# Kernel tuning notes

Hardware: AMD Instinct MI355X
Metric: run time of the kernel (lower is better)

## Reference

```python
import jax, jax.numpy as jnp
import numpy as np

N_A = 100000
N_B = 100000


def _mean_agg(x_src, src, dst, n_dst):
    # gather source features along edges, mean-aggregate into destination nodes
    msgs = x_src[src]                                        # [E, d]
    s = jax.ops.segment_sum(msgs, dst, num_segments=n_dst)   # [n_dst, d]
    ones = jnp.ones((dst.shape[0], 1), dtype=x_src.dtype)
    cnt = jax.ops.segment_sum(ones, dst, num_segments=n_dst)
    return s / jnp.maximum(cnt, jnp.asarray(1.0, x_src.dtype))


def setup_inputs() -> dict:
    key = jax.random.key(0)
    ks = jax.random.split(key, 13)
    E = 1200000
    d = 64
    return {
        "x_A": jax.random.normal(ks[0], (N_A, d), jnp.float32),
        "x_B": jax.random.normal(ks[1], (N_B, d), jnp.float32),
        "Wn": jax.random.normal(ks[2], (2, 3, d, d), jnp.float32) * 0.1,
        "Wr": jax.random.normal(ks[3], (2, 3, d, d), jnp.float32) * 0.1,
        "b": jax.random.normal(ks[4], (2, 3, d), jnp.float32) * 0.1,
        "W_out": jax.random.normal(ks[5], (d, d), jnp.float32) * 0.1,
        "b_out": jax.random.normal(ks[6], (d,), jnp.float32) * 0.1,
        "src0": jax.random.randint(ks[7], (E,), 0, N_A, jnp.int64 if jax.config.jax_enable_x64 else jnp.int32),
        "dst0": jax.random.randint(ks[8], (E,), 0, N_B, jnp.int32),
        "src1": jax.random.randint(ks[9], (E,), 0, N_B, jnp.int32),
        "dst1": jax.random.randint(ks[10], (E,), 0, N_A, jnp.int32),
        "src2": jax.random.randint(ks[11], (E,), 0, N_A, jnp.int32),
        "dst2": jax.random.randint(ks[12], (E,), 0, N_A, jnp.int32),
    }


def reference(x_A, x_B, Wn, Wr, b, W_out, b_out,
              src0, dst0, src1, dst1, src2, dst2):
    # Two stacked heterogeneous conv layers (SAGEConv-style per edge type,
    # summed across edge types per destination node type), then Linear+ReLU head.
    for l in range(2):
        m0 = _mean_agg(x_A, src0, dst0, N_B)  # A -> B
        m1 = _mean_agg(x_B, src1, dst1, N_A)  # B -> A
        m2 = _mean_agg(x_A, src2, dst2, N_A)  # A -> A
        new_B = m0 @ Wn[l, 0] + x_B @ Wr[l, 0] + b[l, 0]
        new_A = (m1 @ Wn[l, 1] + x_A @ Wr[l, 1] + b[l, 1]
                 + m2 @ Wn[l, 2] + x_A @ Wr[l, 2] + b[l, 2])
        x_A, x_B = new_A, new_B
    out_A = jax.nn.relu(x_A @ W_out + b_out)
    out_B = jax.nn.relu(x_B @ W_out + b_out)
    return jnp.concatenate([out_A, out_B], axis=0)  # [N_A + N_B, d]
```

## Files before the change

kernel.cpp:

```cpp
#include <hip/hip_runtime.h>
#include <hip/hip_bf16.h>

typedef __bf16 bf16_t;
typedef unsigned short u16;
typedef short short8 __attribute__((ext_vector_type(8)));
typedef float f32x4 __attribute__((ext_vector_type(4)));

#define BSHIFT 9
#define CAP 8192
#define TILE 4096

__device__ inline short f2bs(float v) {
    bf16_t h = (bf16_t)v;
    return __builtin_bit_cast(short, h);
}
__device__ inline float uif(unsigned u) { return __builtin_bit_cast(float, u); }

__global__ __launch_bounds__(256) void prep_convert(
    const float* __restrict__ xA, const float* __restrict__ xB,
    const float* __restrict__ Wn, const float* __restrict__ Wr,
    const float* __restrict__ Wout,
    u16* __restrict__ plane0, u16* __restrict__ wh, int NA, int NB) {
    int nA4 = NA * 16, nB4 = NB * 16;
    int bA = (nA4 + 255) / 256, bB = (nB4 + 255) / 256;
    int bi = blockIdx.x;
    int tid = threadIdx.x;
    if (bi < bA + bB) {
        const float* in = (bi < bA) ? xA : xB;
        u16* out = (bi < bA) ? plane0 : plane0 + (size_t)NA * 64;
        int i = (bi < bA ? bi : bi - bA) * 256 + tid;
        int n4 = (bi < bA) ? nA4 : nB4;
        if (i >= n4) return;
        float4 v = ((const float4*)in)[i];
        u16 o[4];
        o[0] = (u16)f2bs(v.x); o[1] = (u16)f2bs(v.y);
        o[2] = (u16)f2bs(v.z); o[3] = (u16)f2bs(v.w);
        *(uint2*)(out + (size_t)i * 4) = *(uint2*)o;
        return;
    }
    int mat = bi - bA - bB;
    u16* dstp = wh + (size_t)mat * 4096;
    for (int i = tid; i < 4096; i += 256) {
        int k = i >> 6, n = i & 63;
        float v;
        if (mat < 6) v = Wn[(size_t)mat * 4096 + i];
        else if (mat < 8) v = Wr[(size_t)((mat - 6) * 3 + 0) * 4096 + i];
        else if (mat < 10) v = Wr[(size_t)((mat - 8) * 3 + 1) * 4096 + i]
                             + Wr[(size_t)((mat - 8) * 3 + 2) * 4096 + i];
        else v = Wout[i];
        dstp[n * 64 + k] = (u16)f2bs(v);
    }
}

__global__ __launch_bounds__(256) void init_cursor(int* __restrict__ gcursor, int K) {
    int i = blockIdx.x * 256 + threadIdx.x;
    if (i < K) gcursor[i] = i * CAP;
}

__global__ __launch_bounds__(256) void partition_kernel(
    const int* __restrict__ s0, const int* __restrict__ d0,
    const int* __restrict__ s1, const int* __restrict__ d1,
    const int* __restrict__ s2, const int* __restrict__ d2,
    int* __restrict__ gcursor, int* __restrict__ pairs,
    int NB, int NA, int E, int total) {
    __shared__ int hist[1024];
    __shared__ int gbase[1024];
    int tid = threadIdx.x;
    for (int tile = blockIdx.x * TILE; tile < total; tile += gridDim.x * TILE) {
        for (int i = tid; i < 1024; i += 256) hist[i] = 0;
        __syncthreads();
        int mybkt[16], mypk[16], myrank[16];
#pragma unroll
        for (int j = 0; j < 16; j++) {
            int idx = tile + j * 256 + tid;
            int g = -1, s = 0;
            if (idx < total) {
                if (idx < E) { s = s0[idx]; g = d0[idx]; }
                else if (idx < 2 * E) { s = s1[idx - E]; g = NB + d1[idx - E]; }
                else { s = s2[idx - 2 * E]; g = NB + NA + d2[idx - 2 * E]; }
            }
            if (g >= 0) {
                mybkt[j] = g >> BSHIFT;
                mypk[j] = ((g & ((1 << BSHIFT) - 1)) << 17) | s;
                myrank[j] = atomicAdd(&hist[mybkt[j]], 1);
            } else mybkt[j] = -1;
        }
        __syncthreads();
        for (int bq = tid; bq < 1024; bq += 256) {
            int c = hist[bq];
            if (c) gbase[bq] = atomicAdd(&gcursor[bq], c);
        }
        __syncthreads();
#pragma unroll
        for (int j = 0; j < 16; j++) {
            if (mybkt[j] >= 0)
                pairs[gbase[mybkt[j]] + myrank[j]] = mypk[j];
        }
        __syncthreads();
    }
}

__global__ __launch_bounds__(512) void bucket_fill(const int* __restrict__ pairs,
                                                   const int* __restrict__ gcursor,
                                                   int* __restrict__ off_s,
                                                   int* __restrict__ off_e,
                                                   int* __restrict__ colidx, int M) {
    int b = blockIdx.x;
    int gb = b << BSHIFT;
    __shared__ int cnt[512], cur[512], wsum[8];
    int tid = threadIdx.x;
    int lane = tid & 63, w = tid >> 6;
    int p0 = b * CAP, p1 = gcursor[b];
    cnt[tid] = 0;
    __syncthreads();
    for (int e = p0 + tid; e < p1; e += 512)
        atomicAdd(&cnt[(unsigned)pairs[e] >> 17], 1);
    __syncthreads();
    int v = cnt[tid];
    int x = v;
#pragma unroll
    for (int off = 1; off < 64; off <<= 1) {
        int n = __shfl_up(x, off);
        if (lane >= off) x += n;
    }
    if (lane == 63) wsum[w] = x;
    __syncthreads();
    if (tid == 0) {
        int s = 0;
#pragma unroll
        for (int i = 0; i < 8; i++) { int t = wsum[i]; wsum[i] = s; s += t; }
    }
    __syncthreads();
    int excl = x - v + wsum[w];
    cur[tid] = excl;
    int g = gb + tid;
    if (g < M) { off_s[g] = p0 + excl; off_e[g] = p0 + excl + v; }
    __syncthreads();
    for (int e = p0 + tid; e < p1; e += 512) {
        int p = pairs[e];
        int pos = atomicAdd(&cur[(unsigned)p >> 17], 1);
        colidx[p0 + pos] = p & 0x1FFFF;
    }
}

__device__ __forceinline__ void acc8(uint4 u, f32x4& a0, f32x4& a1) {
    a0[0] += uif(u.x << 16); a0[1] += uif(u.x & 0xFFFF0000u);
    a0[2] += uif(u.y << 16); a0[3] += uif(u.y & 0xFFFF0000u);
    a1[0] += uif(u.z << 16); a1[1] += uif(u.z & 0xFFFF0000u);
    a1[2] += uif(u.w << 16); a1[3] += uif(u.w & 0xFFFF0000u);
}

__global__ __launch_bounds__(256) void gather_all(const u16* __restrict__ plane,
                                                  const int* __restrict__ colidx,
                                                  const int* __restrict__ off_s,
                                                  const int* __restrict__ off_e,
                                                  u16* __restrict__ meanB,
                                                  u16* __restrict__ meanA1,
                                                  u16* __restrict__ meanA2,
                                                  int NB, int NA) {
    int wid = (blockIdx.x * 256 + threadIdx.x) >> 6;
    int lane = threadIdx.x & 63;
    int oct = lane >> 3, fl = lane & 7;
    int M = NB + 2 * NA;
    int grow = wid * 8 + oct;
    if (grow >= M) return;

    const char* tab;
    u16* outp;
    int orow;
    if (grow < NB) { tab = (const char*)plane; outp = meanB; orow = grow; }
    else if (grow < NB + NA) { tab = (const char*)(plane + (size_t)NA * 64); outp = meanA1; orow = grow - NB; }
    else { tab = (const char*)plane; outp = meanA2; orow = grow - NB - NA; }

    int s0 = off_s[grow], s1 = off_e[grow];
    unsigned fo = (unsigned)(fl << 4);
    f32x4 a0 = {0.f, 0.f, 0.f, 0.f}, a1 = {0.f, 0.f, 0.f, 0.f};

    int e = s0;
    if (e + 3 < s1) {
        int c0 = colidx[e], c1 = colidx[e + 1];
        int c2 = colidx[e + 2], c3 = colidx[e + 3];
        while (e + 7 < s1) {
            uint4 u0 = *(const uint4*)(tab + (((unsigned)c0 << 7) | fo));
            uint4 u1 = *(const uint4*)(tab + (((unsigned)c1 << 7) | fo));
            uint4 u2 = *(const uint4*)(tab + (((unsigned)c2 << 7) | fo));
            uint4 u3 = *(const uint4*)(tab + (((unsigned)c3 << 7) | fo));
            c0 = colidx[e + 4]; c1 = colidx[e + 5];
            c2 = colidx[e + 6]; c3 = colidx[e + 7];
            acc8(u0, a0, a1); acc8(u1, a0, a1);
            acc8(u2, a0, a1); acc8(u3, a0, a1);
            e += 4;
        }
        {
            uint4 u0 = *(const uint4*)(tab + (((unsigned)c0 << 7) | fo));
            uint4 u1 = *(const uint4*)(tab + (((unsigned)c1 << 7) | fo));
            uint4 u2 = *(const uint4*)(tab + (((unsigned)c2 << 7) | fo));
            uint4 u3 = *(const uint4*)(tab + (((unsigned)c3 << 7) | fo));
            acc8(u0, a0, a1); acc8(u1, a0, a1);
            acc8(u2, a0, a1); acc8(u3, a0, a1);
            e += 4;
        }
    }
    for (; e < s1; ++e) {
        int c = colidx[e];
        uint4 u = *(const uint4*)(tab + (((unsigned)c << 7) | fo));
        acc8(u, a0, a1);
    }

    float inv = 1.0f / fmaxf((float)(s1 - s0), 1.0f);
    u16 o[8];
#pragma unroll
    for (int i = 0; i < 4; i++) o[i] = (u16)f2bs(a0[i] * inv);
#pragma unroll
    for (int i = 0; i < 4; i++) o[4 + i] = (u16)f2bs(a1[i] * inv);
    *(uint4*)(outp + (size_t)orow * 64 + fl * 8) = *(uint4*)o;
}

template <int NM, int RELU, int OUTF32>
__device__ __forceinline__ void lin_body(
    const u16* __restrict__ m0, const u16* __restrict__ m1,
    const u16* __restrict__ x,
    const u16* __restrict__ Wm0t, const u16* __restrict__ Wm1t,
    const u16* __restrict__ Wxt,
    const float* __restrict__ bias0, const float* __restrict__ bias1,
    void* __restrict__ outv, int nrows, int blk) {
    const int lane = threadIdx.x & 63;
    const int wave = threadIdx.x >> 6;
    const int row0 = blk * 64 + wave * 16;
    if (row0 >= nrows) return;
    const int r = lane & 15;
    const int q = lane >> 4;

    short8 wm0f[2][4], wm1f[2][4], wxf[2][4];
#pragma unroll
    for (int ks = 0; ks < 2; ks++) {
#pragma unroll
        for (int t = 0; t < 4; t++) {
            size_t widx = (size_t)(t * 16 + r) * 64 + ks * 32 + q * 8;
            if (NM >= 1) wm0f[ks][t] = *(const short8*)(Wm0t + widx);
            if (NM >= 2) wm1f[ks][t] = *(const short8*)(Wm1t + widx);
            wxf[ks][t] = *(const short8*)(Wxt + widx);
        }
    }

    f32x4 acc[4];
#pragma unroll
    for (int t = 0; t < 4; t++) {
        float bv = bias0[t * 16 + r];
        if (bias1) bv += bias1[t * 16 + r];
        acc[t][0] = bv; acc[t][1] = bv; acc[t][2] = bv; acc[t][3] = bv;
    }

    const int arow = row0 + r;
    const bool avalid = arow < nrows;
    short8 zf;
#pragma unroll
    for (int j = 0; j < 8; j++) zf[j] = 0;

    if (NM >= 1) {
#pragma unroll
        for (int ks = 0; ks < 2; ks++) {
            short8 af = avalid ? *(const short8*)(m0 + (size_t)arow * 64 + ks * 32 + q * 8) : zf;
#pragma unroll
            for (int t = 0; t < 4; t++)
                acc[t] = __builtin_amdgcn_mfma_f32_16x16x32_bf16(af, wm0f[ks][t], acc[t], 0, 0, 0);
        }
    }
    if (NM >= 2) {
#pragma unroll
        for (int ks = 0; ks < 2; ks++) {
            short8 af = avalid ? *(const short8*)(m1 + (size_t)arow * 64 + ks * 32 + q * 8) : zf;
#pragma unroll
            for (int t = 0; t < 4; t++)
                acc[t] = __builtin_amdgcn_mfma_f32_16x16x32_bf16(af, wm1f[ks][t], acc[t], 0, 0, 0);
        }
    }
#pragma unroll
    for (int ks = 0; ks < 2; ks++) {
        short8 xf = avalid ? *(const short8*)(x + (size_t)arow * 64 + ks * 32 + q * 8) : zf;
#pragma unroll
        for (int t = 0; t < 4; t++)
            acc[t] = __builtin_amdgcn_mfma_f32_16x16x32_bf16(xf, wxf[ks][t], acc[t], 0, 0, 0);
    }

#pragma unroll
    for (int t = 0; t < 4; t++) {
#pragma unroll
        for (int rr = 0; rr < 4; rr++) {
            int row = row0 + q * 4 + rr;
            if (row < nrows) {
                float v = acc[t][rr];
                if (RELU) v = fmaxf(v, 0.0f);
                if (OUTF32) ((float*)outv)[(size_t)row * 64 + t * 16 + r] = v;
                else ((u16*)outv)[(size_t)row * 64 + t * 16 + r] = (u16)f2bs(v);
            }
        }
    }
}

__global__ __launch_bounds__(256) void layer_kernel(
    const u16* __restrict__ plane_in, u16* __restrict__ plane_out,
    const u16* __restrict__ meanB, const u16* __restrict__ meanA1,
    const u16* __restrict__ meanA2, const u16* __restrict__ wh,
    const float* __restrict__ bvec, int l, int NA, int NB, int blocksB) {
    if ((int)blockIdx.x < blocksB) {
        lin_body<1, 0, 0>(meanB, nullptr, plane_in + (size_t)NA * 64,
                          wh + (size_t)(l * 3 + 0) * 4096, nullptr,
                          wh + (size_t)(6 + l) * 4096,
                          bvec + (size_t)(l * 3 + 0) * 64, nullptr,
                          plane_out + (size_t)NA * 64, NB, blockIdx.x);
    } else {
        lin_body<2, 0, 0>(meanA1, meanA2, plane_in,
                          wh + (size_t)(l * 3 + 1) * 4096, wh + (size_t)(l * 3 + 2) * 4096,
                          wh + (size_t)(8 + l) * 4096,
                          bvec + (size_t)(l * 3 + 1) * 64, bvec + (size_t)(l * 3 + 2) * 64,
                          plane_out, NA, blockIdx.x - blocksB);
    }
}

__global__ __launch_bounds__(256) void head_kernel(
    const u16* __restrict__ plane_in, const u16* __restrict__ wh,
    const float* __restrict__ b_out, float* __restrict__ out, int nrows) {
    lin_body<0, 1, 1>(nullptr, nullptr, plane_in,
                      nullptr, nullptr, wh + (size_t)10 * 4096,
                      b_out, nullptr, out, nrows, blockIdx.x);
}

extern "C" void kernel_launch(void* const* d_in, const int* in_sizes, int n_in,
                              void* d_out, int out_size, void* d_ws, size_t ws_size,
                              hipStream_t stream) {
    const float* xA_in = (const float*)d_in[0];
    const float* xB_in = (const float*)d_in[1];
    const float* Wn = (const float*)d_in[2];
    const float* Wr = (const float*)d_in[3];
    const float* b = (const float*)d_in[4];
    const float* W_out = (const float*)d_in[5];
    const float* b_out = (const float*)d_in[6];
    const int* src0 = (const int*)d_in[7];
    const int* dst0 = (const int*)d_in[8];
    const int* src1 = (const int*)d_in[9];
    const int* dst1 = (const int*)d_in[10];
    const int* src2 = (const int*)d_in[11];
    const int* dst2 = (const int*)d_in[12];

    const int NA = in_sizes[0] / 64;
    const int NB = in_sizes[1] / 64;
    const int E = in_sizes[7];
    const int M = NB + NA + NA;
    const int total = 3 * E;
    const int K = (M + (1 << BSHIFT) - 1) >> BSHIFT;

    const size_t PL = (size_t)(NA + NB) * 64;
    u16* plane[2];
    plane[0] = (u16*)d_ws;
    plane[1] = plane[0] + PL;
    u16* wh     = plane[1] + PL;
    u16* meanB  = wh + 11 * 4096;
    u16* meanA1 = meanB + (size_t)NB * 64;
    u16* meanA2 = meanA1 + (size_t)NA * 64;
    int* gcursor= (int*)(meanA2 + (size_t)NA * 64);
    int* off_s  = gcursor + 1024;
    int* off_e  = off_s + M;
    int* colidx = off_e + M;
    int* pairs  = (int*)meanB;

    int bA = (NA * 16 + 255) / 256, bB = (NB * 16 + 255) / 256;
    prep_convert<<<bA + bB + 11, 256, 0, stream>>>(
        xA_in, xB_in, Wn, Wr, W_out, plane[0], wh, NA, NB);

    init_cursor<<<(K + 255) / 256, 256, 0, stream>>>(gcursor, K);
    int ntiles = (total + TILE - 1) / TILE;
    partition_kernel<<<ntiles, 256, 0, stream>>>(src0, dst0, src1, dst1, src2, dst2,
                                                 gcursor, pairs, NB, NA, E, total);
    bucket_fill<<<K, 512, 0, stream>>>(pairs, gcursor, off_s, off_e, colidx, M);

    const int blocksB = (NB + 63) / 64;
    const int blocksA = (NA + 63) / 64;
    int p = 0;
    for (int l = 0; l < 2; l++) {
        gather_all<<<(M + 31) / 32, 256, 0, stream>>>(plane[p], colidx, off_s, off_e,
                                                      meanB, meanA1, meanA2, NB, NA);
        layer_kernel<<<blocksB + blocksA, 256, 0, stream>>>(
            plane[p], plane[1 - p], meanB, meanA1, meanA2, wh, b, l, NA, NB, blocksB);
        p = 1 - p;
    }

    head_kernel<<<(NA + NB + 63) / 64, 256, 0, stream>>>(
        plane[p], wh, b_out, (float*)d_out, NA + NB);
}
```

Before: 427.2 us.

## Fuse head into layer-2 kernel, merge cursor init, widen partition blocks

The output head linear+ReLU now runs inside the second layer kernel. Each wave writes its layer-2 tile to shared memory and applies W_out right there, so the full bf16 plane is neither written to nor re-read from global memory, and one launch is removed. Cursor initialisation is folded into prep_convert as an extra block, which drops another launch. The partition kernel now uses 1024-thread blocks with larger tiles, one histogram bin per thread. Weight fragments are loaded inline inside the MFMA loop instead of being preloaded, which changes register pressure and load scheduling.

```diff
diff --git a/kernel.cpp b/kernel.cpp
--- a/kernel.cpp
+++ b/kernel.cpp
@@ -8,7 +8,7 @@
 
 #define BSHIFT 9
 #define CAP 8192
-#define TILE 4096
+#define TILE 16384
 
 __device__ inline short f2bs(float v) {
     bf16_t h = (bf16_t)v;
@@ -20,7 +20,8 @@
     const float* __restrict__ xA, const float* __restrict__ xB,
     const float* __restrict__ Wn, const float* __restrict__ Wr,
     const float* __restrict__ Wout,
-    u16* __restrict__ plane0, u16* __restrict__ wh, int NA, int NB) {
+    u16* __restrict__ plane0, u16* __restrict__ wh,
+    int* __restrict__ gcursor, int NA, int NB, int K) {
     int nA4 = NA * 16, nB4 = NB * 16;
     int bA = (nA4 + 255) / 256, bB = (nB4 + 255) / 256;
     int bi = blockIdx.x;
@@ -38,26 +39,25 @@
         *(uint2*)(out + (size_t)i * 4) = *(uint2*)o;
         return;
     }
-    int mat = bi - bA - bB;
-    u16* dstp = wh + (size_t)mat * 4096;
-    for (int i = tid; i < 4096; i += 256) {
-        int k = i >> 6, n = i & 63;
-        float v;
-        if (mat < 6) v = Wn[(size_t)mat * 4096 + i];
-        else if (mat < 8) v = Wr[(size_t)((mat - 6) * 3 + 0) * 4096 + i];
-        else if (mat < 10) v = Wr[(size_t)((mat - 8) * 3 + 1) * 4096 + i]
-                             + Wr[(size_t)((mat - 8) * 3 + 2) * 4096 + i];
-        else v = Wout[i];
-        dstp[n * 64 + k] = (u16)f2bs(v);
-    }
-}
-
-__global__ __launch_bounds__(256) void init_cursor(int* __restrict__ gcursor, int K) {
-    int i = blockIdx.x * 256 + threadIdx.x;
-    if (i < K) gcursor[i] = i * CAP;
-}
-
-__global__ __launch_bounds__(256) void partition_kernel(
+    if (bi < bA + bB + 11) {
+        int mat = bi - bA - bB;
+        u16* dstp = wh + (size_t)mat * 4096;
+        for (int i = tid; i < 4096; i += 256) {
+            int k = i >> 6, n = i & 63;
+            float v;
+            if (mat < 6) v = Wn[(size_t)mat * 4096 + i];
+            else if (mat < 8) v = Wr[(size_t)((mat - 6) * 3 + 0) * 4096 + i];
+            else if (mat < 10) v = Wr[(size_t)((mat - 8) * 3 + 1) * 4096 + i]
+                                 + Wr[(size_t)((mat - 8) * 3 + 2) * 4096 + i];
+            else v = Wout[i];
+            dstp[n * 64 + k] = (u16)f2bs(v);
+        }
+        return;
+    }
+    for (int i = tid; i < K; i += 256) gcursor[i] = i * CAP;
+}
+
+__global__ __launch_bounds__(1024) void partition_kernel(
     const int* __restrict__ s0, const int* __restrict__ d0,
     const int* __restrict__ s1, const int* __restrict__ d1,
     const int* __restrict__ s2, const int* __restrict__ d2,
@@ -67,12 +67,12 @@
     __shared__ int gbase[1024];
     int tid = threadIdx.x;
     for (int tile = blockIdx.x * TILE; tile < total; tile += gridDim.x * TILE) {
-        for (int i = tid; i < 1024; i += 256) hist[i] = 0;
+        hist[tid] = 0;
         __syncthreads();
         int mybkt[16], mypk[16], myrank[16];
 #pragma unroll
         for (int j = 0; j < 16; j++) {
-            int idx = tile + j * 256 + tid;
+            int idx = tile + j * 1024 + tid;
             int g = -1, s = 0;
             if (idx < total) {
                 if (idx < E) { s = s0[idx]; g = d0[idx]; }
@@ -86,9 +86,9 @@
             } else mybkt[j] = -1;
         }
         __syncthreads();
-        for (int bq = tid; bq < 1024; bq += 256) {
-            int c = hist[bq];
-            if (c) gbase[bq] = atomicAdd(&gcursor[bq], c);
+        {
+            int c = hist[tid];
+            if (c) gbase[tid] = atomicAdd(&gcursor[tid], c);
         }
         __syncthreads();
 #pragma unroll
@@ -216,14 +216,15 @@
     *(uint4*)(outp + (size_t)orow * 64 + fl * 8) = *(uint4*)o;
 }
 
-template <int NM, int RELU, int OUTF32>
+
+template <int NM>
 __device__ __forceinline__ void lin_body(
     const u16* __restrict__ m0, const u16* __restrict__ m1,
     const u16* __restrict__ x,
     const u16* __restrict__ Wm0t, const u16* __restrict__ Wm1t,
     const u16* __restrict__ Wxt,
     const float* __restrict__ bias0, const float* __restrict__ bias1,
-    void* __restrict__ outv, int nrows, int blk) {
+    u16* __restrict__ outv, int nrows, int blk) {
     const int lane = threadIdx.x & 63;
     const int wave = threadIdx.x >> 6;
     const int row0 = blk * 64 + wave * 16;
@@ -231,23 +232,11 @@
     const int r = lane & 15;
     const int q = lane >> 4;
 
-    short8 wm0f[2][4], wm1f[2][4], wxf[2][4];
-#pragma unroll
-    for (int ks = 0; ks < 2; ks++) {
-#pragma unroll
-        for (int t = 0; t < 4; t++) {
-            size_t widx = (size_t)(t * 16 + r) * 64 + ks * 32 + q * 8;
-            if (NM >= 1) wm0f[ks][t] = *(const short8*)(Wm0t + widx);
-            if (NM >= 2) wm1f[ks][t] = *(const short8*)(Wm1t + widx);
-            wxf[ks][t] = *(const short8*)(Wxt + widx);
-        }
-    }
-
     f32x4 acc[4];
 #pragma unroll
     for (int t = 0; t < 4; t++) {
         float bv = bias0[t * 16 + r];
-        if (bias1) bv += bias1[t * 16 + r];
+        if (NM >= 2) bv += bias1[t * 16 + r];
         acc[t][0] = bv; acc[t][1] = bv; acc[t][2] = bv; acc[t][3] = bv;
     }
 
@@ -257,30 +246,20 @@
 #pragma unroll
     for (int j = 0; j < 8; j++) zf[j] = 0;
 
-    if (NM >= 1) {
-#pragma unroll
-        for (int ks = 0; ks < 2; ks++) {
-            short8 af = avalid ? *(const short8*)(m0 + (size_t)arow * 64 + ks * 32 + q * 8) : zf;
-#pragma unroll
-            for (int t = 0; t < 4; t++)
-                acc[t] = __builtin_amdgcn_mfma_f32_16x16x32_bf16(af, wm0f[ks][t], acc[t], 0, 0, 0);
-        }
-    }
-    if (NM >= 2) {
-#pragma unroll
-        for (int ks = 0; ks < 2; ks++) {
-            short8 af = avalid ? *(const short8*)(m1 + (size_t)arow * 64 + ks * 32 + q * 8) : zf;
-#pragma unroll
-            for (int t = 0; t < 4; t++)
-                acc[t] = __builtin_amdgcn_mfma_f32_16x16x32_bf16(af, wm1f[ks][t], acc[t], 0, 0, 0);
-        }
-    }
 #pragma unroll
     for (int ks = 0; ks < 2; ks++) {
+        short8 af = avalid ? *(const short8*)(m0 + (size_t)arow * 64 + ks * 32 + q * 8) : zf;
         short8 xf = avalid ? *(const short8*)(x + (size_t)arow * 64 + ks * 32 + q * 8) : zf;
-#pragma unroll
-        for (int t = 0; t < 4; t++)
-            acc[t] = __builtin_amdgcn_mfma_f32_16x16x32_bf16(xf, wxf[ks][t], acc[t], 0, 0, 0);
+        short8 bf_;
+        if (NM >= 2) bf_ = avalid ? *(const short8*)(m1 + (size_t)arow * 64 + ks * 32 + q * 8) : zf;
+#pragma unroll
+        for (int t = 0; t < 4; t++) {
+            size_t widx = (size_t)(t * 16 + r) * 64 + ks * 32 + q * 8;
+            acc[t] = __builtin_amdgcn_mfma_f32_16x16x32_bf16(af, *(const short8*)(Wm0t + widx), acc[t], 0, 0, 0);
+            if (NM >= 2)
+                acc[t] = __builtin_amdgcn_mfma_f32_16x16x32_bf16(bf_, *(const short8*)(Wm1t + widx), acc[t], 0, 0, 0);
+            acc[t] = __builtin_amdgcn_mfma_f32_16x16x32_bf16(xf, *(const short8*)(Wxt + widx), acc[t], 0, 0, 0);
+        }
     }
 
 #pragma unroll
@@ -288,42 +267,128 @@
 #pragma unroll
         for (int rr = 0; rr < 4; rr++) {
             int row = row0 + q * 4 + rr;
-            if (row < nrows) {
-                float v = acc[t][rr];
-                if (RELU) v = fmaxf(v, 0.0f);
-                if (OUTF32) ((float*)outv)[(size_t)row * 64 + t * 16 + r] = v;
-                else ((u16*)outv)[(size_t)row * 64 + t * 16 + r] = (u16)f2bs(v);
-            }
-        }
-    }
-}
-
-__global__ __launch_bounds__(256) void layer_kernel(
+            if (row < nrows)
+                outv[(size_t)row * 64 + t * 16 + r] = (u16)f2bs(acc[t][rr]);
+        }
+    }
+}
+
+__global__ __launch_bounds__(256) void layer1_kernel(
     const u16* __restrict__ plane_in, u16* __restrict__ plane_out,
     const u16* __restrict__ meanB, const u16* __restrict__ meanA1,
     const u16* __restrict__ meanA2, const u16* __restrict__ wh,
-    const float* __restrict__ bvec, int l, int NA, int NB, int blocksB) {
+    const float* __restrict__ bvec, int NA, int NB, int blocksB) {
     if ((int)blockIdx.x < blocksB) {
-        lin_body<1, 0, 0>(meanB, nullptr, plane_in + (size_t)NA * 64,
-                          wh + (size_t)(l * 3 + 0) * 4096, nullptr,
-                          wh + (size_t)(6 + l) * 4096,
-                          bvec + (size_t)(l * 3 + 0) * 64, nullptr,
-                          plane_out + (size_t)NA * 64, NB, blockIdx.x);
+        lin_body<1>(meanB, nullptr, plane_in + (size_t)NA * 64,
+                    wh + (size_t)0 * 4096, nullptr, wh + (size_t)6 * 4096,
+                    bvec + (size_t)0 * 64, nullptr,
+                    plane_out + (size_t)NA * 64, NB, blockIdx.x);
     } else {
-        lin_body<2, 0, 0>(meanA1, meanA2, plane_in,
-                          wh + (size_t)(l * 3 + 1) * 4096, wh + (size_t)(l * 3 + 2) * 4096,
-                          wh + (size_t)(8 + l) * 4096,
-                          bvec + (size_t)(l * 3 + 1) * 64, bvec + (size_t)(l * 3 + 2) * 64,
-                          plane_out, NA, blockIdx.x - blocksB);
-    }
-}
-
-__global__ __launch_bounds__(256) void head_kernel(
-    const u16* __restrict__ plane_in, const u16* __restrict__ wh,
-    const float* __restrict__ b_out, float* __restrict__ out, int nrows) {
-    lin_body<0, 1, 1>(nullptr, nullptr, plane_in,
-                      nullptr, nullptr, wh + (size_t)10 * 4096,
-                      b_out, nullptr, out, nrows, blockIdx.x);
+        lin_body<2>(meanA1, meanA2, plane_in,
+                    wh + (size_t)1 * 4096, wh + (size_t)2 * 4096, wh + (size_t)8 * 4096,
+                    bvec + (size_t)1 * 64, bvec + (size_t)2 * 64,
+                    plane_out, NA, blockIdx.x - blocksB);
+    }
+}
+
+template <int NM>
+__device__ __forceinline__ void lin_body_head(
+    const u16* __restrict__ m0, const u16* __restrict__ m1,
+    const u16* __restrict__ x,
+    const u16* __restrict__ Wm0t, const u16* __restrict__ Wm1t,
+    const u16* __restrict__ Wxt,
+    const float* __restrict__ bias0, const float* __restrict__ bias1,
+    const u16* __restrict__ Woutt, const float* __restrict__ b_out,
+    float* __restrict__ out, int nrows, int blk) {
+    const int lane = threadIdx.x & 63;
+    const int wave = threadIdx.x >> 6;
+    const int row0 = blk * 64 + wave * 16;
+    const int r = lane & 15;
+    const int q = lane >> 4;
+    const int arow = row0 + r;
+    const bool avalid = (row0 < nrows) && (arow < nrows);
+
+    __shared__ __align__(16) u16 xt[4][16][72];
+
+    f32x4 acc[4];
+#pragma unroll
+    for (int t = 0; t < 4; t++) {
+        float bv = bias0[t * 16 + r];
+        if (NM >= 2) bv += bias1[t * 16 + r];
+        acc[t][0] = bv; acc[t][1] = bv; acc[t][2] = bv; acc[t][3] = bv;
+    }
+
+    short8 zf;
+#pragma unroll
+    for (int j = 0; j < 8; j++) zf[j] = 0;
+
+#pragma unroll
+    for (int ks = 0; ks < 2; ks++) {
+        short8 af = avalid ? *(const short8*)(m0 + (size_t)arow * 64 + ks * 32 + q * 8) : zf;
+        short8 xf = avalid ? *(const short8*)(x + (size_t)arow * 64 + ks * 32 + q * 8) : zf;
+        short8 bf_;
+        if (NM >= 2) bf_ = avalid ? *(const short8*)(m1 + (size_t)arow * 64 + ks * 32 + q * 8) : zf;
+#pragma unroll
+        for (int t = 0; t < 4; t++) {
+            size_t widx = (size_t)(t * 16 + r) * 64 + ks * 32 + q * 8;
+            acc[t] = __builtin_amdgcn_mfma_f32_16x16x32_bf16(af, *(const short8*)(Wm0t + widx), acc[t], 0, 0, 0);
+            if (NM >= 2)
+                acc[t] = __builtin_amdgcn_mfma_f32_16x16x32_bf16(bf_, *(const short8*)(Wm1t + widx), acc[t], 0, 0, 0);
+            acc[t] = __builtin_amdgcn_mfma_f32_16x16x32_bf16(xf, *(const short8*)(Wxt + widx), acc[t], 0, 0, 0);
+        }
+    }
+
+#pragma unroll
+    for (int t = 0; t < 4; t++)
+#pragma unroll
+        for (int rr = 0; rr < 4; rr++)
+            xt[wave][q * 4 + rr][t * 16 + r] = (u16)f2bs(acc[t][rr]);
+    __syncthreads();
+
+    f32x4 hacc[4];
+#pragma unroll
+    for (int t = 0; t < 4; t++) {
+        float bv = b_out[t * 16 + r];
+        hacc[t][0] = bv; hacc[t][1] = bv; hacc[t][2] = bv; hacc[t][3] = bv;
+    }
+#pragma unroll
+    for (int ks = 0; ks < 2; ks++) {
+        short8 yf = *(const short8*)&xt[wave][r][ks * 32 + q * 8];
+#pragma unroll
+        for (int t = 0; t < 4; t++) {
+            size_t widx = (size_t)(t * 16 + r) * 64 + ks * 32 + q * 8;
+            hacc[t] = __builtin_amdgcn_mfma_f32_16x16x32_bf16(yf, *(const short8*)(Woutt + widx), hacc[t], 0, 0, 0);
+        }
+    }
+#pragma unroll
+    for (int t = 0; t < 4; t++) {
+#pragma unroll
+        for (int rr = 0; rr < 4; rr++) {
+            int row = row0 + q * 4 + rr;
+            if (row < nrows)
+                out[(size_t)row * 64 + t * 16 + r] = fmaxf(hacc[t][rr], 0.0f);
+        }
+    }
+}
+
+__global__ __launch_bounds__(256) void layer2_head_kernel(
+    const u16* __restrict__ plane_in,
+    const u16* __restrict__ meanB, const u16* __restrict__ meanA1,
+    const u16* __restrict__ meanA2, const u16* __restrict__ wh,
+    const float* __restrict__ bvec, const float* __restrict__ b_out,
+    float* __restrict__ out, int NA, int NB, int blocksB) {
+    const u16* Woutt = wh + (size_t)10 * 4096;
+    if ((int)blockIdx.x < blocksB) {
+        lin_body_head<1>(meanB, nullptr, plane_in + (size_t)NA * 64,
+                         wh + (size_t)3 * 4096, nullptr, wh + (size_t)7 * 4096,
+                         bvec + (size_t)3 * 64, nullptr,
+                         Woutt, b_out, out + (size_t)NA * 64, NB, blockIdx.x);
+    } else {
+        lin_body_head<2>(meanA1, meanA2, plane_in,
+                         wh + (size_t)4 * 4096, wh + (size_t)5 * 4096, wh + (size_t)9 * 4096,
+                         bvec + (size_t)4 * 64, bvec + (size_t)5 * 64,
+                         Woutt, b_out, out, NA, blockIdx.x - blocksB);
+    }
 }
 
 extern "C" void kernel_launch(void* const* d_in, const int* in_sizes, int n_in,
@@ -365,26 +430,23 @@
     int* pairs  = (int*)meanB;
 
     int bA = (NA * 16 + 255) / 256, bB = (NB * 16 + 255) / 256;
-    prep_convert<<<bA + bB + 11, 256, 0, stream>>>(
-        xA_in, xB_in, Wn, Wr, W_out, plane[0], wh, NA, NB);
-
-    init_cursor<<<(K + 255) / 256, 256, 0, stream>>>(gcursor, K);
+    prep_convert<<<bA + bB + 11 + 1, 256, 0, stream>>>(
+        xA_in, xB_in, Wn, Wr, W_out, plane[0], wh, gcursor, NA, NB, K);
+
     int ntiles = (total + TILE - 1) / TILE;
-    partition_kernel<<<ntiles, 256, 0, stream>>>(src0, dst0, src1, dst1, src2, dst2,
-                                                 gcursor, pairs, NB, NA, E, total);
+    partition_kernel<<<ntiles, 1024, 0, stream>>>(src0, dst0, src1, dst1, src2, dst2,
+                                                  gcursor, pairs, NB, NA, E, total);
     bucket_fill<<<K, 512, 0, stream>>>(pairs, gcursor, off_s, off_e, colidx, M);
 
     const int blocksB = (NB + 63) / 64;
     const int blocksA = (NA + 63) / 64;
-    int p = 0;
-    for (int l = 0; l < 2; l++) {
-        gather_all<<<(M + 31) / 32, 256, 0, stream>>>(plane[p], colidx, off_s, off_e,
-                                                      meanB, meanA1, meanA2, NB, NA);
-        layer_kernel<<<blocksB + blocksA, 256, 0, stream>>>(
-            plane[p], plane[1 - p], meanB, meanA1, meanA2, wh, b, l, NA, NB, blocksB);
-        p = 1 - p;
-    }
-
-    head_kernel<<<(NA + NB + 63) / 64, 256, 0, stream>>>(
-        plane[p], wh, b_out, (float*)d_out, NA + NB);
-}
+    gather_all<<<(M + 31) / 32, 256, 0, stream>>>(plane[0], colidx, off_s, off_e,
+                                                  meanB, meanA1, meanA2, NB, NA);
+    layer1_kernel<<<blocksB + blocksA, 256, 0, stream>>>(
+        plane[0], plane[1], meanB, meanA1, meanA2, wh, b, NA, NB, blocksB);
+
+    gather_all<<<(M + 31) / 32, 256, 0, stream>>>(plane[1], colidx, off_s, off_e,
+                                                  meanB, meanA1, meanA2, NB, NA);
+    layer2_head_kernel<<<blocksB + blocksA, 256, 0, stream>>>(
+        plane[1], meanB, meanA1, meanA2, wh, b, b_out, (float*)d_out, NA, NB, blocksB);
+}
```

Result: faster. 414.4 us (-3.0%).

## Fold output head into layer-2 weights and fuse init into prep kernel

Applied to the files above, without the earlier changes.

Precomputes the products of the layer-2 weights with W_out and the matching combined biases, so the second layer writes the ReLU head output directly and the separate head kernel and its intermediate plane round trip go away. The cursor init and bias folding move into the prep kernel, which removes one launch. The partition kernel switches to 1024-thread blocks with larger tiles, and lin_body now loads weight fragments inside the MFMA loop instead of preloading them into registers. The folded weights are rounded to bf16 after the product, which shifts numerics slightly.

```diff
diff --git a/kernel.cpp b/kernel.cpp
--- a/kernel.cpp
+++ b/kernel.cpp
@@ -8,7 +8,7 @@
 
 #define BSHIFT 9
 #define CAP 8192
-#define TILE 4096
+#define TILE 16384
 
 __device__ inline short f2bs(float v) {
     bf16_t h = (bf16_t)v;
@@ -19,8 +19,11 @@
 __global__ __launch_bounds__(256) void prep_convert(
     const float* __restrict__ xA, const float* __restrict__ xB,
     const float* __restrict__ Wn, const float* __restrict__ Wr,
-    const float* __restrict__ Wout,
-    u16* __restrict__ plane0, u16* __restrict__ wh, int NA, int NB) {
+    const float* __restrict__ Wout, const float* __restrict__ b,
+    const float* __restrict__ b_out,
+    u16* __restrict__ plane0, u16* __restrict__ wh,
+    int* __restrict__ gcursor, float* __restrict__ biasC,
+    int NA, int NB, int K) {
     int nA4 = NA * 16, nB4 = NB * 16;
     int bA = (nA4 + 255) / 256, bB = (nB4 + 255) / 256;
     int bi = blockIdx.x;
@@ -38,26 +41,60 @@
         *(uint2*)(out + (size_t)i * 4) = *(uint2*)o;
         return;
     }
-    int mat = bi - bA - bB;
-    u16* dstp = wh + (size_t)mat * 4096;
-    for (int i = tid; i < 4096; i += 256) {
-        int k = i >> 6, n = i & 63;
-        float v;
-        if (mat < 6) v = Wn[(size_t)mat * 4096 + i];
-        else if (mat < 8) v = Wr[(size_t)((mat - 6) * 3 + 0) * 4096 + i];
-        else if (mat < 10) v = Wr[(size_t)((mat - 8) * 3 + 1) * 4096 + i]
-                             + Wr[(size_t)((mat - 8) * 3 + 2) * 4096 + i];
-        else v = Wout[i];
-        dstp[n * 64 + k] = (u16)f2bs(v);
-    }
-}
-
-__global__ __launch_bounds__(256) void init_cursor(int* __restrict__ gcursor, int K) {
-    int i = blockIdx.x * 256 + threadIdx.x;
-    if (i < K) gcursor[i] = i * CAP;
-}
-
-__global__ __launch_bounds__(256) void partition_kernel(
+    if (bi < bA + bB + 11) {
+        int mat = bi - bA - bB;
+        u16* dstp = wh + (size_t)mat * 4096;
+        for (int i = tid; i < 4096; i += 256) {
+            int k = i >> 6, n = i & 63;
+            float v;
+            if (mat < 6) v = Wn[(size_t)mat * 4096 + i];
+            else if (mat < 8) v = Wr[(size_t)((mat - 6) * 3 + 0) * 4096 + i];
+            else if (mat < 10) v = Wr[(size_t)((mat - 8) * 3 + 1) * 4096 + i]
+                                 + Wr[(size_t)((mat - 8) * 3 + 2) * 4096 + i];
+            else v = Wout[i];
+            dstp[n * 64 + k] = (u16)f2bs(v);
+        }
+        return;
+    }
+    if (bi < bA + bB + 11 + 5) {
+        int c = bi - bA - bB - 11;
+        const float* Wsrc;
+        const float* Wsrc2 = nullptr;
+        if (c == 0) Wsrc = Wn + (size_t)3 * 4096;
+        else if (c == 1) Wsrc = Wr + (size_t)3 * 4096;
+        else if (c == 2) Wsrc = Wn + (size_t)4 * 4096;
+        else if (c == 3) Wsrc = Wn + (size_t)5 * 4096;
+        else { Wsrc = Wr + (size_t)4 * 4096; Wsrc2 = Wr + (size_t)5 * 4096; }
+        u16* dstp = wh + (size_t)(11 + c) * 4096;
+        for (int i = tid; i < 4096; i += 256) {
+            int k = i >> 6, n = i & 63;
+            float s = 0.f;
+            for (int j = 0; j < 64; j++) {
+                float w = Wsrc[k * 64 + j];
+                if (Wsrc2) w += Wsrc2[k * 64 + j];
+                s += w * Wout[j * 64 + n];
+            }
+            dstp[n * 64 + k] = (u16)f2bs(s);
+        }
+        return;
+    }
+    for (int i = tid; i < K; i += 256) gcursor[i] = i * CAP;
+    if (tid < 64) {
+        int n = tid;
+        float s0 = b_out[n], s1 = b_out[n];
+        for (int j = 0; j < 64; j++) {
+            float wo = Wout[j * 64 + n];
+            s0 += b[3 * 64 + j] * wo;
+            s1 += (b[4 * 64 + j] + b[5 * 64 + j]) * wo;
+        }
+        biasC[0 * 64 + n] = b[0 * 64 + n];
+        biasC[1 * 64 + n] = b[1 * 64 + n] + b[2 * 64 + n];
+        biasC[2 * 64 + n] = s0;
+        biasC[3 * 64 + n] = s1;
+    }
+}
+
+__global__ __launch_bounds__(1024) void partition_kernel(
     const int* __restrict__ s0, const int* __restrict__ d0,
     const int* __restrict__ s1, const int* __restrict__ d1,
     const int* __restrict__ s2, const int* __restrict__ d2,
@@ -67,12 +104,12 @@
     __shared__ int gbase[1024];
     int tid = threadIdx.x;
     for (int tile = blockIdx.x * TILE; tile < total; tile += gridDim.x * TILE) {
-        for (int i = tid; i < 1024; i += 256) hist[i] = 0;
+        hist[tid] = 0;
         __syncthreads();
         int mybkt[16], mypk[16], myrank[16];
 #pragma unroll
         for (int j = 0; j < 16; j++) {
-            int idx = tile + j * 256 + tid;
+            int idx = tile + j * 1024 + tid;
             int g = -1, s = 0;
             if (idx < total) {
                 if (idx < E) { s = s0[idx]; g = d0[idx]; }
@@ -86,9 +123,9 @@
             } else mybkt[j] = -1;
         }
         __syncthreads();
-        for (int bq = tid; bq < 1024; bq += 256) {
-            int c = hist[bq];
-            if (c) gbase[bq] = atomicAdd(&gcursor[bq], c);
+        {
+            int c = hist[tid];
+            if (c) gbase[tid] = atomicAdd(&gcursor[tid], c);
         }
         __syncthreads();
 #pragma unroll
@@ -222,7 +259,7 @@
     const u16* __restrict__ x,
     const u16* __restrict__ Wm0t, const u16* __restrict__ Wm1t,
     const u16* __restrict__ Wxt,
-    const float* __restrict__ bias0, const float* __restrict__ bias1,
+    const float* __restrict__ bias64,
     void* __restrict__ outv, int nrows, int blk) {
     const int lane = threadIdx.x & 63;
     const int wave = threadIdx.x >> 6;
@@ -231,23 +268,10 @@
     const int r = lane & 15;
     const int q = lane >> 4;
 
-    short8 wm0f[2][4], wm1f[2][4], wxf[2][4];
-#pragma unroll
-    for (int ks = 0; ks < 2; ks++) {
-#pragma unroll
-        for (int t = 0; t < 4; t++) {
-            size_t widx = (size_t)(t * 16 + r) * 64 + ks * 32 + q * 8;
-            if (NM >= 1) wm0f[ks][t] = *(const short8*)(Wm0t + widx);
-            if (NM >= 2) wm1f[ks][t] = *(const short8*)(Wm1t + widx);
-            wxf[ks][t] = *(const short8*)(Wxt + widx);
-        }
-    }
-
     f32x4 acc[4];
 #pragma unroll
     for (int t = 0; t < 4; t++) {
-        float bv = bias0[t * 16 + r];
-        if (bias1) bv += bias1[t * 16 + r];
+        float bv = bias64[t * 16 + r];
         acc[t][0] = bv; acc[t][1] = bv; acc[t][2] = bv; acc[t][3] = bv;
     }
 
@@ -257,30 +281,20 @@
 #pragma unroll
     for (int j = 0; j < 8; j++) zf[j] = 0;
 
-    if (NM >= 1) {
-#pragma unroll
-        for (int ks = 0; ks < 2; ks++) {
-            short8 af = avalid ? *(const short8*)(m0 + (size_t)arow * 64 + ks * 32 + q * 8) : zf;
-#pragma unroll
-            for (int t = 0; t < 4; t++)
-                acc[t] = __builtin_amdgcn_mfma_f32_16x16x32_bf16(af, wm0f[ks][t], acc[t], 0, 0, 0);
-        }
-    }
-    if (NM >= 2) {
-#pragma unroll
-        for (int ks = 0; ks < 2; ks++) {
-            short8 af = avalid ? *(const short8*)(m1 + (size_t)arow * 64 + ks * 32 + q * 8) : zf;
-#pragma unroll
-            for (int t = 0; t < 4; t++)
-                acc[t] = __builtin_amdgcn_mfma_f32_16x16x32_bf16(af, wm1f[ks][t], acc[t], 0, 0, 0);
-        }
-    }
 #pragma unroll
     for (int ks = 0; ks < 2; ks++) {
+        short8 af = avalid ? *(const short8*)(m0 + (size_t)arow * 64 + ks * 32 + q * 8) : zf;
         short8 xf = avalid ? *(const short8*)(x + (size_t)arow * 64 + ks * 32 + q * 8) : zf;
-#pragma unroll
-        for (int t = 0; t < 4; t++)
-            acc[t] = __builtin_amdgcn_mfma_f32_16x16x32_bf16(xf, wxf[ks][t], acc[t], 0, 0, 0);
+        short8 bf_;
+        if (NM >= 2) bf_ = avalid ? *(const short8*)(m1 + (size_t)arow * 64 + ks * 32 + q * 8) : zf;
+#pragma unroll
+        for (int t = 0; t < 4; t++) {
+            size_t widx = (size_t)(t * 16 + r) * 64 + ks * 32 + q * 8;
+            acc[t] = __builtin_amdgcn_mfma_f32_16x16x32_bf16(af, *(const short8*)(Wm0t + widx), acc[t], 0, 0, 0);
+            if (NM >= 2)
+                acc[t] = __builtin_amdgcn_mfma_f32_16x16x32_bf16(bf_, *(const short8*)(Wm1t + widx), acc[t], 0, 0, 0);
+            acc[t] = __builtin_amdgcn_mfma_f32_16x16x32_bf16(xf, *(const short8*)(Wxt + widx), acc[t], 0, 0, 0);
+        }
     }
 
 #pragma unroll
@@ -291,39 +305,50 @@
             if (row < nrows) {
                 float v = acc[t][rr];
                 if (RELU) v = fmaxf(v, 0.0f);
-                if (OUTF32) ((float*)outv)[(size_t)row * 64 + t * 16 + r] = v;
-                else ((u16*)outv)[(size_t)row * 64 + t * 16 + r] = (u16)f2bs(v);
+                if (OUTF32)
+                    __builtin_nontemporal_store(v, (float*)outv + (size_t)row * 64 + t * 16 + r);
+                else
+                    ((u16*)outv)[(size_t)row * 64 + t * 16 + r] = (u16)f2bs(v);
             }
         }
     }
 }
 
-__global__ __launch_bounds__(256) void layer_kernel(
+__global__ __launch_bounds__(256) void layer1_kernel(
     const u16* __restrict__ plane_in, u16* __restrict__ plane_out,
     const u16* __restrict__ meanB, const u16* __restrict__ meanA1,
     const u16* __restrict__ meanA2, const u16* __restrict__ wh,
-    const float* __restrict__ bvec, int l, int NA, int NB, int blocksB) {
+    const float* __restrict__ biasC, int NA, int NB, int blocksB) {
     if ((int)blockIdx.x < blocksB) {
         lin_body<1, 0, 0>(meanB, nullptr, plane_in + (size_t)NA * 64,
-                          wh + (size_t)(l * 3 + 0) * 4096, nullptr,
-                          wh + (size_t)(6 + l) * 4096,
-                          bvec + (size_t)(l * 3 + 0) * 64, nullptr,
+                          wh + (size_t)0 * 4096, nullptr, wh + (size_t)6 * 4096,
+                          biasC + 0 * 64,
                           plane_out + (size_t)NA * 64, NB, blockIdx.x);
     } else {
         lin_body<2, 0, 0>(meanA1, meanA2, plane_in,
-                          wh + (size_t)(l * 3 + 1) * 4096, wh + (size_t)(l * 3 + 2) * 4096,
-                          wh + (size_t)(8 + l) * 4096,
-                          bvec + (size_t)(l * 3 + 1) * 64, bvec + (size_t)(l * 3 + 2) * 64,
+                          wh + (size_t)1 * 4096, wh + (size_t)2 * 4096, wh + (size_t)8 * 4096,
+                          biasC + 1 * 64,
                           plane_out, NA, blockIdx.x - blocksB);
     }
 }
 
-__global__ __launch_bounds__(256) void head_kernel(
-    const u16* __restrict__ plane_in, const u16* __restrict__ wh,
-    const float* __restrict__ b_out, float* __restrict__ out, int nrows) {
-    lin_body<0, 1, 1>(nullptr, nullptr, plane_in,
-                      nullptr, nullptr, wh + (size_t)10 * 4096,
-                      b_out, nullptr, out, nrows, blockIdx.x);
+__global__ __launch_bounds__(256) void layer2_head_kernel(
+    const u16* __restrict__ plane_in,
+    const u16* __restrict__ meanB, const u16* __restrict__ meanA1,
+    const u16* __restrict__ meanA2, const u16* __restrict__ wh,
+    const float* __restrict__ biasC,
+    float* __restrict__ out, int NA, int NB, int blocksB) {
+    if ((int)blockIdx.x < blocksB) {
+        lin_body<1, 1, 1>(meanB, nullptr, plane_in + (size_t)NA * 64,
+                          wh + (size_t)11 * 4096, nullptr, wh + (size_t)12 * 4096,
+                          biasC + 2 * 64,
+                          out + (size_t)NA * 64, NB, blockIdx.x);
+    } else {
+        lin_body<2, 1, 1>(meanA1, meanA2, plane_in,
+                          wh + (size_t)13 * 4096, wh + (size_t)14 * 4096, wh + (size_t)15 * 4096,
+                          biasC + 3 * 64,
+                          out, NA, blockIdx.x - blocksB);
+    }
 }
 
 extern "C" void kernel_launch(void* const* d_in, const int* in_sizes, int n_in,
@@ -355,36 +380,35 @@
     plane[0] = (u16*)d_ws;
     plane[1] = plane[0] + PL;
     u16* wh     = plane[1] + PL;
-    u16* meanB  = wh + 11 * 4096;
+    u16* meanB  = wh + 16 * 4096;
     u16* meanA1 = meanB + (size_t)NB * 64;
     u16* meanA2 = meanA1 + (size_t)NA * 64;
     int* gcursor= (int*)(meanA2 + (size_t)NA * 64);
-    int* off_s  = gcursor + 1024;
+    float* biasC= (float*)(gcursor + 1024);
+    int* off_s  = (int*)(biasC + 256);
     int* off_e  = off_s + M;
     int* colidx = off_e + M;
     int* pairs  = (int*)meanB;
 
     int bA = (NA * 16 + 255) / 256, bB = (NB * 16 + 255) / 256;
-    prep_convert<<<bA + bB + 11, 256, 0, stream>>>(
-        xA_in, xB_in, Wn, Wr, W_out, plane[0], wh, NA, NB);
-
-    init_cursor<<<(K + 255) / 256, 256, 0, stream>>>(gcursor, K);
+    prep_convert<<<bA + bB + 11 + 5 + 1, 256, 0, stream>>>(
+        xA_in, xB_in, Wn, Wr, W_out, b, b_out,
+        plane[0], wh, gcursor, biasC, NA, NB, K);
+
     int ntiles = (total + TILE - 1) / TILE;
-    partition_kernel<<<ntiles, 256, 0, stream>>>(src0, dst0, src1, dst1, src2, dst2,
-                                                 gcursor, pairs, NB, NA, E, total);
+    partition_kernel<<<ntiles, 1024, 0, stream>>>(src0, dst0, src1, dst1, src2, dst2,
+                                                  gcursor, pairs, NB, NA, E, total);
     bucket_fill<<<K, 512, 0, stream>>>(pairs, gcursor, off_s, off_e, colidx, M);
 
     const int blocksB = (NB + 63) / 64;
     const int blocksA = (NA + 63) / 64;
-    int p = 0;
-    for (int l = 0; l < 2; l++) {
-        gather_all<<<(M + 31) / 32, 256, 0, stream>>>(plane[p], colidx, off_s, off_e,
-                                                      meanB, meanA1, meanA2, NB, NA);
-        layer_kernel<<<blocksB + blocksA, 256, 0, stream>>>(
-            plane[p], plane[1 - p], meanB, meanA1, meanA2, wh, b, l, NA, NB, blocksB);
-        p = 1 - p;
-    }
-
-    head_kernel<<<(NA + NB + 63) / 64, 256, 0, stream>>>(
-        plane[p], wh, b_out, (float*)d_out, NA + NB);
-}
+    gather_all<<<(M + 31) / 32, 256, 0, stream>>>(plane[0], colidx, off_s, off_e,
+                                                  meanB, meanA1, meanA2, NB, NA);
+    layer1_kernel<<<blocksB + blocksA, 256, 0, stream>>>(
+        plane[0], plane[1], meanB, meanA1, meanA2, wh, biasC, NA, NB, blocksB);
+
+    gather_all<<<(M + 31) / 32, 256, 0, stream>>>(plane[1], colidx, off_s, off_e,
+                                                  meanB, meanA1, meanA2, NB, NA);
+    layer2_head_kernel<<<blocksB + blocksA, 256, 0, stream>>>(
+        plane[1], meanB, meanA1, meanA2, wh, biasC, (float*)d_out, NA, NB, blocksB);
+}
```

Result: slower. 518.7 us (+21.4%).
